# Kernel tuning notes

Measured on AMD Instinct MI355X. Metric: run time of the kernel, lower is better.

## Reference

```python
import jax, jax.numpy as jnp
import numpy as np

EPS = 1e-12

def _l2norm(v, axis=-1):
    return v / jnp.sqrt(jnp.sum(v * v, axis=axis, keepdims=True) + EPS)

def setup_inputs() -> dict:
    key = jax.random.key(0)
    k1, k2, k3 = jax.random.split(key, 3)
    B, D, C, K = 8192, 1024, 90, 16
    x = jax.random.normal(k1, (B, D), dtype=jnp.float32)
    labels = jax.random.randint(k2, (B,), 0, C, dtype=jnp.int64)
    centers = jax.random.normal(k3, (C, K, D), dtype=jnp.float32)
    return {"x": x, "labels": labels, "centers": centers}

def reference(x, labels, centers):
    # l2Norm branch of CenterWoParamMultiCosineLoss (cosine distances).
    # centers are normalized at init; x is normalized in forward.
    xn = _l2norm(x)                              # [B, D]
    cn = _l2norm(centers)                        # [C, K, D]
    c = cn[labels]                               # [B, K, D] gather per label
    # inner cosine distances per center: d_k = 1 - x . c_k
    d = 1.0 - jnp.einsum('bd,bkd->bk', xn, c)    # [B, K]
    # detached normalized scores
    dd = jax.lax.stop_gradient(d)
    score = dd / jnp.sum(dd, axis=1, keepdims=True)  # [B, K]
    # K > 1 with l2Norm: weight each distance by (1 - score)
    per_sample = jnp.sum((1.0 - score) * d, axis=1)  # [B]
    return jnp.mean(per_sample)
```

## Files before the change

### kernel.cpp

```cpp
#include <hip/hip_runtime.h>

#define EPS 1e-12f

constexpr int D       = 1024;
constexpr int K       = 16;
constexpr int NS      = 16;
constexpr int BATCH   = 16;
constexpr int LISTCAP = 512;

__global__ __launch_bounds__(256) void cosine_loss_fused(
    const float* __restrict__ x, const int* __restrict__ labels,
    const float* __restrict__ centers, float* __restrict__ out,
    int B, int C, float inv_B) {
    const int bid  = blockIdx.x;
    const int c    = bid % C;
    const int sl   = bid / C;
    const int tid  = threadIdx.x;
    const int w    = tid >> 6;
    const int lane = tid & 63;

    __shared__ int   list[LISTCAP];
    __shared__ int   wsum[4];
    __shared__ float dotsLDS[BATCH][K + 1];
    __shared__ float xxLDS[BATCH];
    __shared__ float cinvLDS[K];
    __shared__ float accLDS;

    const int SLICE = (B + NS - 1) / NS;
    const int base  = sl * SLICE;
    const int lim   = min(SLICE, B - base);
    const int rpt   = (SLICE + 255) >> 8;

    int mmask = 0, cnt_t = 0;
    for (int r = 0; r < rpt; ++r) {
        const int idx = r * 256 + tid;
        if (idx < lim && labels[base + idx] == c) { mmask |= 1 << r; ++cnt_t; }
    }

    int v = cnt_t;
#pragma unroll
    for (int off = 1; off < 64; off <<= 1) {
        const int u = __shfl_up(v, off, 64);
        if (lane >= off) v += u;
    }
    if (lane == 63) wsum[w] = v;
    __syncthreads();
    int prefix = 0;
#pragma unroll
    for (int ww = 0; ww < 4; ++ww) if (ww < w) prefix += wsum[ww];
    const int cnt = wsum[0] + wsum[1] + wsum[2] + wsum[3];

    int pos = prefix + v - cnt_t;
    for (int r = 0; r < rpt; ++r) {
        if ((mmask >> r) & 1) list[pos++] = base + r * 256 + tid;
    }
    if (tid == 0) accLDS = 0.0f;
    __syncthreads();

    const int kbase = 4 * w;
    float4 cf[4][4];
    float  cc[4] = {0.f, 0.f, 0.f, 0.f};
#pragma unroll
    for (int kk = 0; kk < 4; ++kk) {
        const float* crow = centers + (size_t)(c * K + kbase + kk) * D;
#pragma unroll
        for (int j = 0; j < 4; ++j) {
            float4 t = *reinterpret_cast<const float4*>(crow + j * 256 + lane * 4);
            cf[kk][j] = t;
            cc[kk] += t.x * t.x + t.y * t.y + t.z * t.z + t.w * t.w;
        }
    }
#pragma unroll
    for (int off = 32; off >= 1; off >>= 1) {
#pragma unroll
        for (int kk = 0; kk < 4; ++kk) cc[kk] += __shfl_xor(cc[kk], off, 64);
    }
    if (lane == 0) {
#pragma unroll
        for (int kk = 0; kk < 4; ++kk)
            cinvLDS[kbase + kk] = 1.0f / sqrtf(cc[kk] + EPS);
    }

    float4 xf[4], xfn[4];
    if (cnt > 0) {
        const float* xrow = x + (size_t)list[0] * D;
#pragma unroll
        for (int j = 0; j < 4; ++j)
            xf[j] = *reinterpret_cast<const float4*>(xrow + j * 256 + lane * 4);
    }
    for (int si = 0; si < cnt; ++si) {
        if (si + 1 < cnt) {
            const float* xrow = x + (size_t)list[si + 1] * D;
#pragma unroll
            for (int j = 0; j < 4; ++j)
                xfn[j] = *reinterpret_cast<const float4*>(xrow + j * 256 + lane * 4);
        }
        float acc[4] = {0.f, 0.f, 0.f, 0.f};
        float xx = 0.f;
#pragma unroll
        for (int j = 0; j < 4; ++j) {
#pragma unroll
            for (int kk = 0; kk < 4; ++kk) {
                acc[kk] += cf[kk][j].x * xf[j].x + cf[kk][j].y * xf[j].y +
                           cf[kk][j].z * xf[j].z + cf[kk][j].w * xf[j].w;
            }
            if (w == 0)
                xx += xf[j].x * xf[j].x + xf[j].y * xf[j].y +
                      xf[j].z * xf[j].z + xf[j].w * xf[j].w;
        }
#pragma unroll
        for (int off = 32; off >= 1; off >>= 1) {
#pragma unroll
            for (int kk = 0; kk < 4; ++kk) acc[kk] += __shfl_xor(acc[kk], off, 64);
            if (w == 0) xx += __shfl_xor(xx, off, 64);
        }
        const int slot = si & (BATCH - 1);
        if (lane == 0) {
#pragma unroll
            for (int kk = 0; kk < 4; ++kk) dotsLDS[slot][kbase + kk] = acc[kk];
            if (w == 0) xxLDS[slot] = xx;
        }
#pragma unroll
        for (int j = 0; j < 4; ++j) xf[j] = xfn[j];

        if (slot == BATCH - 1 || si + 1 == cnt) {
            __syncthreads();
            const int bl = slot + 1;
            if (tid < 64) {
                float per = 0.f;
                if (tid < bl) {
                    const float nxinv = 1.0f / sqrtf(xxLDS[tid] + EPS);
                    float sum_d = 0.f, sum_d2 = 0.f;
#pragma unroll
                    for (int k = 0; k < K; ++k) {
                        const float dk = 1.0f - dotsLDS[tid][k] * nxinv * cinvLDS[k];
                        sum_d  += dk;
                        sum_d2 += dk * dk;
                    }
                    per = sum_d - sum_d2 / sum_d;
                }
#pragma unroll
                for (int off = 32; off >= 1; off >>= 1)
                    per += __shfl_xor(per, off, 64);
                if (tid == 0) accLDS += per;
            }
            __syncthreads();
        }
    }

    __syncthreads();
    if (tid == 0 && cnt > 0) atomicAdd(out, accLDS * inv_B);
}

extern "C" void kernel_launch(void* const* d_in, const int* in_sizes, int n_in,
                              void* d_out, int out_size, void* d_ws, size_t ws_size,
                              hipStream_t stream) {
    const float* x       = (const float*)d_in[0];
    const int*   labels  = (const int*)d_in[1];
    const float* centers = (const float*)d_in[2];

    const int B = in_sizes[1];
    const int C = in_sizes[2] / (K * D);
    const int nblocks = C * NS;

    float* out = (float*)d_out;

    hipMemsetAsync(out, 0, sizeof(float), stream);

    cosine_loss_fused<<<nblocks, 256, 0, stream>>>(
        x, labels, centers, out, B, C, 1.0f / (float)B);
}
```

Before: 104.7 us.

## Stage class centers in LDS and give each wave whole sample pairs

Result: slower. 258.3 us (+146.8%).

```diff
diff --git a/kernel.cpp b/kernel.cpp
--- a/kernel.cpp
+++ b/kernel.cpp
@@ -4,11 +4,10 @@
 
 constexpr int D       = 1024;
 constexpr int K       = 16;
-constexpr int NS      = 16;
-constexpr int BATCH   = 16;
-constexpr int LISTCAP = 512;
+constexpr int NS      = 8;
+constexpr int LISTCAP = 1024;
 
-__global__ __launch_bounds__(256) void cosine_loss_fused(
+__global__ __launch_bounds__(256, 2) void cosine_loss_fused(
     const float* __restrict__ x, const int* __restrict__ labels,
     const float* __restrict__ centers, float* __restrict__ out,
     int B, int C, float inv_B) {
@@ -19,17 +18,26 @@
     const int w    = tid >> 6;
     const int lane = tid & 63;
 
+    __shared__ float cLDS[K * D];
     __shared__ int   list[LISTCAP];
-    __shared__ int   wsum[4];
-    __shared__ float dotsLDS[BATCH][K + 1];
-    __shared__ float xxLDS[BATCH];
+    __shared__ int   wsumI[4];
     __shared__ float cinvLDS[K];
-    __shared__ float accLDS;
+    __shared__ float wpart[4];
 
     const int SLICE = (B + NS - 1) / NS;
     const int base  = sl * SLICE;
     const int lim   = min(SLICE, B - base);
     const int rpt   = (SLICE + 255) >> 8;
+
+    {
+        const float* csrc = centers + (size_t)c * (K * D);
+#pragma unroll
+        for (int i = 0; i < (K * D) / (256 * 4); ++i) {
+            const int off = (i * 256 + tid) * 4;
+            const float4 t = *reinterpret_cast<const float4*>(csrc + off);
+            *reinterpret_cast<float4*>(&cLDS[off]) = t;
+        }
+    }
 
     int mmask = 0, cnt_t = 0;
     for (int r = 0; r < rpt; ++r) {
@@ -43,113 +51,127 @@
         const int u = __shfl_up(v, off, 64);
         if (lane >= off) v += u;
     }
-    if (lane == 63) wsum[w] = v;
+    if (lane == 63) wsumI[w] = v;
     __syncthreads();
     int prefix = 0;
 #pragma unroll
-    for (int ww = 0; ww < 4; ++ww) if (ww < w) prefix += wsum[ww];
-    const int cnt = wsum[0] + wsum[1] + wsum[2] + wsum[3];
+    for (int ww = 0; ww < 4; ++ww) if (ww < w) prefix += wsumI[ww];
+    const int cnt = wsumI[0] + wsumI[1] + wsumI[2] + wsumI[3];
 
     int pos = prefix + v - cnt_t;
     for (int r = 0; r < rpt; ++r) {
         if ((mmask >> r) & 1) list[pos++] = base + r * 256 + tid;
     }
-    if (tid == 0) accLDS = 0.0f;
-    __syncthreads();
 
-    const int kbase = 4 * w;
-    float4 cf[4][4];
-    float  cc[4] = {0.f, 0.f, 0.f, 0.f};
+    {
+        float cc[4] = {0.f, 0.f, 0.f, 0.f};
 #pragma unroll
-    for (int kk = 0; kk < 4; ++kk) {
-        const float* crow = centers + (size_t)(c * K + kbase + kk) * D;
+        for (int kk = 0; kk < 4; ++kk) {
 #pragma unroll
-        for (int j = 0; j < 4; ++j) {
-            float4 t = *reinterpret_cast<const float4*>(crow + j * 256 + lane * 4);
-            cf[kk][j] = t;
-            cc[kk] += t.x * t.x + t.y * t.y + t.z * t.z + t.w * t.w;
-        }
-    }
-#pragma unroll
-    for (int off = 32; off >= 1; off >>= 1) {
-#pragma unroll
-        for (int kk = 0; kk < 4; ++kk) cc[kk] += __shfl_xor(cc[kk], off, 64);
-    }
-    if (lane == 0) {
-#pragma unroll
-        for (int kk = 0; kk < 4; ++kk)
-            cinvLDS[kbase + kk] = 1.0f / sqrtf(cc[kk] + EPS);
-    }
-
-    float4 xf[4], xfn[4];
-    if (cnt > 0) {
-        const float* xrow = x + (size_t)list[0] * D;
-#pragma unroll
-        for (int j = 0; j < 4; ++j)
-            xf[j] = *reinterpret_cast<const float4*>(xrow + j * 256 + lane * 4);
-    }
-    for (int si = 0; si < cnt; ++si) {
-        if (si + 1 < cnt) {
-            const float* xrow = x + (size_t)list[si + 1] * D;
-#pragma unroll
-            for (int j = 0; j < 4; ++j)
-                xfn[j] = *reinterpret_cast<const float4*>(xrow + j * 256 + lane * 4);
-        }
-        float acc[4] = {0.f, 0.f, 0.f, 0.f};
-        float xx = 0.f;
-#pragma unroll
-        for (int j = 0; j < 4; ++j) {
-#pragma unroll
-            for (int kk = 0; kk < 4; ++kk) {
-                acc[kk] += cf[kk][j].x * xf[j].x + cf[kk][j].y * xf[j].y +
-                           cf[kk][j].z * xf[j].z + cf[kk][j].w * xf[j].w;
+            for (int j = 0; j < 4; ++j) {
+                const float4 t = *reinterpret_cast<const float4*>(
+                    &cLDS[(4 * w + kk) * D + j * 256 + lane * 4]);
+                cc[kk] += t.x * t.x + t.y * t.y + t.z * t.z + t.w * t.w;
             }
-            if (w == 0)
-                xx += xf[j].x * xf[j].x + xf[j].y * xf[j].y +
-                      xf[j].z * xf[j].z + xf[j].w * xf[j].w;
         }
 #pragma unroll
         for (int off = 32; off >= 1; off >>= 1) {
 #pragma unroll
-            for (int kk = 0; kk < 4; ++kk) acc[kk] += __shfl_xor(acc[kk], off, 64);
-            if (w == 0) xx += __shfl_xor(xx, off, 64);
+            for (int kk = 0; kk < 4; ++kk) cc[kk] += __shfl_xor(cc[kk], off, 64);
         }
-        const int slot = si & (BATCH - 1);
         if (lane == 0) {
 #pragma unroll
-            for (int kk = 0; kk < 4; ++kk) dotsLDS[slot][kbase + kk] = acc[kk];
-            if (w == 0) xxLDS[slot] = xx;
+            for (int kk = 0; kk < 4; ++kk)
+                cinvLDS[4 * w + kk] = 1.0f / sqrtf(cc[kk] + EPS);
         }
+    }
+    __syncthreads();
+
+    float cinv_r[K];
 #pragma unroll
-        for (int j = 0; j < 4; ++j) xf[j] = xfn[j];
+    for (int k = 0; k < K; ++k) cinv_r[k] = cinvLDS[k];
 
-        if (slot == BATCH - 1 || si + 1 == cnt) {
-            __syncthreads();
-            const int bl = slot + 1;
-            if (tid < 64) {
-                float per = 0.f;
-                if (tid < bl) {
-                    const float nxinv = 1.0f / sqrtf(xxLDS[tid] + EPS);
-                    float sum_d = 0.f, sum_d2 = 0.f;
+    float wacc = 0.0f;
+    const int npairs = (cnt + 1) >> 1;
+    for (int t = w; t < npairs; t += 4) {
+        const int  i1v = 2 * t + 1;
+        const bool v1  = (i1v < cnt);
+        const int  s0  = list[2 * t];
+        const int  s1  = v1 ? list[i1v] : s0;
+
+        const float* xr0 = x + (size_t)s0 * D;
+        const float* xr1 = x + (size_t)s1 * D;
+        float4 xa[4], xb[4];
 #pragma unroll
-                    for (int k = 0; k < K; ++k) {
-                        const float dk = 1.0f - dotsLDS[tid][k] * nxinv * cinvLDS[k];
-                        sum_d  += dk;
-                        sum_d2 += dk * dk;
-                    }
-                    per = sum_d - sum_d2 / sum_d;
+        for (int j = 0; j < 4; ++j) {
+            xa[j] = *reinterpret_cast<const float4*>(xr0 + j * 256 + lane * 4);
+            xb[j] = *reinterpret_cast<const float4*>(xr1 + j * 256 + lane * 4);
+        }
+
+        float aa[K], ab[K];
+#pragma unroll
+        for (int k = 0; k < K; ++k) { aa[k] = 0.f; ab[k] = 0.f; }
+        float xxa = 0.f, xxb = 0.f;
+#pragma unroll
+        for (int j = 0; j < 4; ++j) {
+            xxa += xa[j].x * xa[j].x + xa[j].y * xa[j].y +
+                   xa[j].z * xa[j].z + xa[j].w * xa[j].w;
+            xxb += xb[j].x * xb[j].x + xb[j].y * xb[j].y +
+                   xb[j].z * xb[j].z + xb[j].w * xb[j].w;
+#pragma unroll
+            for (int k = 0; k < K; ++k) {
+                const float4 ck = *reinterpret_cast<const float4*>(
+                    &cLDS[k * D + j * 256 + lane * 4]);
+                aa[k] += ck.x * xa[j].x + ck.y * xa[j].y +
+                         ck.z * xa[j].z + ck.w * xa[j].w;
+                ab[k] += ck.x * xb[j].x + ck.y * xb[j].y +
+                         ck.z * xb[j].z + ck.w * xb[j].w;
+            }
+        }
+
+#pragma unroll
+        for (int off = 32; off >= 1; off >>= 1) {
+#pragma unroll
+            for (int k = 0; k < K; ++k) {
+                aa[k] += __shfl_xor(aa[k], off, 64);
+                ab[k] += __shfl_xor(ab[k], off, 64);
+            }
+            xxa += __shfl_xor(xxa, off, 64);
+            xxb += __shfl_xor(xxb, off, 64);
+        }
+
+        if (lane == 0) {
+            {
+                const float n0 = 1.0f / sqrtf(xxa + EPS);
+                float sd = 0.f, sd2 = 0.f;
+#pragma unroll
+                for (int k = 0; k < K; ++k) {
+                    const float dk = 1.0f - aa[k] * n0 * cinv_r[k];
+                    sd  += dk;
+                    sd2 += dk * dk;
                 }
+                wacc += sd - sd2 / sd;
+            }
+            if (v1) {
+                const float n1 = 1.0f / sqrtf(xxb + EPS);
+                float sd = 0.f, sd2 = 0.f;
 #pragma unroll
-                for (int off = 32; off >= 1; off >>= 1)
-                    per += __shfl_xor(per, off, 64);
-                if (tid == 0) accLDS += per;
+                for (int k = 0; k < K; ++k) {
+                    const float dk = 1.0f - ab[k] * n1 * cinv_r[k];
+                    sd  += dk;
+                    sd2 += dk * dk;
+                }
+                wacc += sd - sd2 / sd;
             }
-            __syncthreads();
         }
     }
 
+    if (lane == 0) wpart[w] = wacc;
     __syncthreads();
-    if (tid == 0 && cnt > 0) atomicAdd(out, accLDS * inv_B);
+    if (tid == 0) {
+        const float bsum = (wpart[0] + wpart[1]) + (wpart[2] + wpart[3]);
+        atomicAdd(out, bsum * inv_B);
+    }
 }
 
 extern "C" void kernel_launch(void* const* d_in, const int* in_sizes, int n_in,
```
